# Kernel optimization log

Hardware: AMD Instinct MI355X
Metric: run time of the kernel (lower is better)

## Reference

```python
import jax, jax.numpy as jnp
import numpy as np

NUM_HEADS = 16
DIM_HEAD = 64
MAX_LEN = 512


def setup_inputs() -> dict:
    key = jax.random.key(0)
    ks = jax.random.split(key, 6)
    B, N, D = 16, 512, 1024
    inner = NUM_HEADS * DIM_HEAD  # 1024
    x = jax.random.normal(ks[0], (B, N, D), dtype=jnp.float32)
    w_qkv = jax.random.normal(ks[1], (D, 3 * inner), dtype=jnp.float32) * (D ** -0.5)
    b_qkv = jnp.zeros((3 * inner,), dtype=jnp.float32)
    rel_emb = jax.random.normal(ks[2], (2 * MAX_LEN - 1, NUM_HEADS), dtype=jnp.float32) * 0.02
    w_out = jax.random.normal(ks[3], (inner, D), dtype=jnp.float32) * (inner ** -0.5)
    b_out = jnp.zeros((D,), dtype=jnp.float32)
    return {"x": x, "w_qkv": w_qkv, "b_qkv": b_qkv, "rel_emb": rel_emb,
            "w_out": w_out, "b_out": b_out}


def reference(x, w_qkv, b_qkv, rel_emb, w_out, b_out):
    B, N, D = x.shape
    h, dh = NUM_HEADS, DIM_HEAD
    scale = dh ** -0.5
    qkv = x @ w_qkv + b_qkv  # (B, N, 3*h*dh)
    q, k, v = jnp.split(qkv, 3, axis=-1)
    def to_heads(t):
        return t.reshape(B, N, h, dh).transpose(0, 2, 1, 3)  # (B, h, N, dh)
    q, k, v = to_heads(q), to_heads(k), to_heads(v)
    dots = jnp.einsum('bhid,bhjd->bhij', q, k) * scale  # (B, h, N, N)
    # relative position bias: emb[(i - j) + max_len - 1] -> (N, N, h) -> (1, h, N, N)
    idx = jnp.arange(N)[:, None] - jnp.arange(N)[None, :] + (MAX_LEN - 1)
    bias = rel_emb[idx].transpose(2, 0, 1)[None]  # (1, h, N, N)
    attn = jax.nn.softmax(dots + bias, axis=-1)
    out = jnp.einsum('bhij,bhjd->bhid', attn, v)  # (B, h, N, dh)
    out = out.transpose(0, 2, 1, 3).reshape(B, N, h * dh)
    return out @ w_out + b_out
```

## Files before the change

### kernel.cpp

```cpp
#include <hip/hip_runtime.h>

#define SEQ    512
#define NH     16
#define DH     64
#define DMODEL 1024
#define NB     16
#define MROWS  (NB*SEQ)
#define MAXL   512

typedef _Float16 f16;
typedef f16  f16x8 __attribute__((ext_vector_type(8)));
typedef f16  f16x4 __attribute__((ext_vector_type(4)));
typedef float f32x4 __attribute__((ext_vector_type(4)));

__device__ static inline void gll16(const f16* g, f16* l) {
    __builtin_amdgcn_global_load_lds(
        (const __attribute__((address_space(1))) void*)(g),
        (__attribute__((address_space(3))) void*)(l), 16, 0, 0);
}

__global__ __launch_bounds__(256)
void prep(const float* __restrict__ x, f16* __restrict__ xh,
          const float* __restrict__ wqkv, f16* __restrict__ wqkvT,
          const float* __restrict__ wout, f16* __restrict__ woutT)
{
    const int bid = blockIdx.x, t = threadIdx.x;
    if (bid < 8192) {
        int i = (bid * 256 + t) * 4;
        float4 v = *(const float4*)(x + i);
        f16x4 h = { (f16)v.x, (f16)v.y, (f16)v.z, (f16)v.w };
        *(f16x4*)(xh + i) = h;
        return;
    }
    __shared__ float tile[32][33];
    const float* in; f16* out; int C, gx, gy;
    if (bid < 8192 + 3072) {
        int b2 = bid - 8192; in = wqkv; out = wqkvT; C = 3072;
        gx = b2 % 96; gy = b2 / 96;
    } else {
        int b2 = bid - 11264; in = wout; out = woutT; C = 1024;
        gx = b2 & 31; gy = b2 >> 5;
    }
    const int R = 1024;
    int tx = t & 31, ty = t >> 5;
    int c0 = gx * 32, r0 = gy * 32;
    #pragma unroll
    for (int i = 0; i < 4; ++i)
        tile[ty + i * 8][tx] = in[(size_t)(r0 + ty + i * 8) * C + c0 + tx];
    __syncthreads();
    #pragma unroll
    for (int i = 0; i < 4; ++i)
        out[(size_t)(c0 + ty + i * 8) * R + r0 + tx] = (f16)tile[tx][ty + i * 8];
}

template<int MODE>
__global__ __launch_bounds__(256)
void gemm_mfma(const f16* __restrict__ A, const f16* __restrict__ Bt,
               const float* __restrict__ bias, int N, int K,
               float* __restrict__ Cout,
               f16* __restrict__ qb, f16* __restrict__ kb, f16* __restrict__ vb)
{
    __shared__ f16 As[128 * 64];
    __shared__ f16 Bs[128 * 64];
    const int t = threadIdx.x;
    const int lane = t & 63, w = t >> 6;
    const int quad = lane >> 4, l16 = lane & 15;
    const int xr = l16 & 7;
    const int m0 = blockIdx.y * 128, n0 = blockIdx.x * 128;
    const int wm = (w & 1) * 64, wn = (w >> 1) * 64;

    f32x4 acc[4][4];
    #pragma unroll
    for (int i = 0; i < 4; ++i)
        #pragma unroll
        for (int j = 0; j < 4; ++j)
            acc[i][j] = f32x4{0.f, 0.f, 0.f, 0.f};

    const int sr8 = lane >> 3;
    const int sc8 = (lane & 7) ^ sr8;
    const f16* agp = A  + (size_t)(m0 + w * 32 + sr8) * K + sc8 * 8;
    const f16* bgp = Bt + (size_t)(n0 + w * 32 + sr8) * K + sc8 * 8;
    f16* asl = As + w * 2048;
    f16* bsl = Bs + w * 2048;

    for (int k0 = 0; k0 < K; k0 += 64) {
        __syncthreads();
        #pragma unroll
        for (int c = 0; c < 4; ++c) {
            gll16(agp + k0 + c * 8 * K, asl + c * 512);
            gll16(bgp + k0 + c * 8 * K, bsl + c * 512);
        }
        __syncthreads();
        #pragma unroll
        for (int ks = 0; ks < 2; ++ks) {
            f16x8 af[4], bf[4];
            #pragma unroll
            for (int ms = 0; ms < 4; ++ms)
                af[ms] = *(const f16x8*)&As[(wm + ms * 16 + l16) * 64
                                            + (((ks * 4 + quad) ^ xr) * 8)];
            #pragma unroll
            for (int ns = 0; ns < 4; ++ns)
                bf[ns] = *(const f16x8*)&Bs[(wn + ns * 16 + l16) * 64
                                            + (((ks * 4 + quad) ^ xr) * 8)];
            #pragma unroll
            for (int ms = 0; ms < 4; ++ms)
                #pragma unroll
                for (int ns = 0; ns < 4; ++ns)
                    acc[ms][ns] = __builtin_amdgcn_mfma_f32_16x16x32_f16(
                        af[ms], bf[ns], acc[ms][ns], 0, 0, 0);
        }
    }

    if (MODE == 0) {
        #pragma unroll
        for (int ns = 0; ns < 4; ++ns) {
            int col = n0 + wn + ns * 16 + l16;
            float bv = bias[col];
            int which = col >> 10;
            int hh = (col & 1023) >> 6, d = col & 63;
            #pragma unroll
            for (int ms = 0; ms < 4; ++ms) {
                int rowb = m0 + wm + ms * 16 + quad * 4;
                int bb_ = rowb >> 9, n_ = rowb & 511;
                if (which == 0) {
                    #pragma unroll
                    for (int reg = 0; reg < 4; ++reg)
                        qb[((size_t)(bb_ * NH + hh) * SEQ + n_ + reg) * DH + d] =
                            (f16)(acc[ms][ns][reg] + bv);
                } else if (which == 2) {
                    f16x4 pk;
                    #pragma unroll
                    for (int reg = 0; reg < 4; ++reg)
                        pk[reg] = (f16)(acc[ms][ns][reg] + bv);
                    int c8s = ((n_ >> 3) & 7) ^ (d & 7);
                    *(f16x4*)(vb + ((size_t)(bb_ * NH + hh) * DH + d) * SEQ
                                 + (n_ & ~63) + c8s * 8 + (n_ & 7)) = pk;
                } else {
                    #pragma unroll
                    for (int reg = 0; reg < 4; ++reg) {
                        int n = n_ + reg;
                        int dd = (((d >> 3) ^ (n & 7)) * 8) + (d & 7);
                        kb[((size_t)(bb_ * NH + hh) * SEQ + n) * DH + dd] =
                            (f16)(acc[ms][ns][reg] + bv);
                    }
                }
            }
        }
    } else {
        #pragma unroll
        for (int ns = 0; ns < 4; ++ns) {
            int col = n0 + wn + ns * 16 + l16;
            float bv = bias[col];
            #pragma unroll
            for (int ms = 0; ms < 4; ++ms) {
                int rowb = m0 + wm + ms * 16 + quad * 4;
                #pragma unroll
                for (int reg = 0; reg < 4; ++reg)
                    Cout[(size_t)(rowb + reg) * N + col] = acc[ms][ns][reg] + bv;
            }
        }
    }
}

__global__ __launch_bounds__(512)
void attn_mfma(const f16* __restrict__ qb, const f16* __restrict__ kb,
               const f16* __restrict__ vb, const float* __restrict__ rel,
               f16* __restrict__ ob)
{
    __shared__ f16 Ks[128 * 64];
    __shared__ f16 Vt[64 * 128];
    __shared__ f16 Pw[8][16 * 64];
    __shared__ float relh[1024];

    const int t = threadIdx.x;
    const int lane = t & 63, w = t >> 6;
    const int quad = lane >> 4, l16 = lane & 15;
    const int xr = l16 & 7;
    const int bh = blockIdx.x;
    const int h = bh & 15, b = bh >> 4;

    for (int i = t; i < 2 * MAXL - 1; i += 512)
        relh[i] = rel[i * NH + h] * 1.44269504f;

    f16x8 qf[4][2];
    #pragma unroll
    for (int c = 0; c < 4; ++c) {
        const f16* qrow = qb + ((size_t)bh * SEQ + w * 64 + c * 16 + l16) * DH + quad * 8;
        qf[c][0] = *(const f16x8*)(qrow);
        qf[c][1] = *(const f16x8*)(qrow + 32);
    }

    f32x4 o[4][4];
    float lsum[4];
    #pragma unroll
    for (int c = 0; c < 4; ++c) {
        lsum[c] = 0.f;
        #pragma unroll
        for (int dt = 0; dt < 4; ++dt) o[c][dt] = f32x4{0.f, 0.f, 0.f, 0.f};
    }

    const f16* kbase = kb + (size_t)bh * SEQ * DH;
    const f16* vbase = vb + (size_t)bh * DH * SEQ;
    f16* pw = &Pw[w][0];

    for (int kt = 0; kt < 4; ++kt) {
        __syncthreads();
        #pragma unroll
        for (int r = 0; r < 2; ++r) {
            const f16* src = kbase + (size_t)(kt * 128 + r * 64 + w * 8 + (lane >> 3)) * DH
                           + (lane & 7) * 8;
            gll16(src, Ks + r * 4096 + w * 512);
        }
        #pragma unroll
        for (int r = 0; r < 2; ++r) {
            const f16* src = vbase + (size_t)(r * 32 + w * 4 + (lane >> 4)) * SEQ
                           + kt * 128 + ((lane & 15) >> 3) * 64 + (lane & 7) * 8;
            gll16(src, Vt + r * 4096 + w * 512);
        }
        __syncthreads();

        #pragma unroll
        for (int c = 0; c < 4; ++c) {
            f32x4 sT[8];
            #pragma unroll
            for (int mt = 0; mt < 8; ++mt) {
                const f16* kr = &Ks[(mt * 16 + l16) * 64];
                f16x8 a0 = *(const f16x8*)(kr + ((quad ^ xr) * 8));
                f16x8 a1 = *(const f16x8*)(kr + (((4 + quad) ^ xr) * 8));
                f32x4 s = f32x4{0.f, 0.f, 0.f, 0.f};
                s = __builtin_amdgcn_mfma_f32_16x16x32_f16(a0, qf[c][0], s, 0, 0, 0);
                s = __builtin_amdgcn_mfma_f32_16x16x32_f16(a1, qf[c][1], s, 0, 0, 0);
                sT[mt] = s;
            }

            const int cb0 = w * 64 + c * 16 + l16 + (MAXL - 1) - kt * 128 - quad * 4;
            #pragma unroll
            for (int g = 0; g < 2; ++g) {
                #pragma unroll
                for (int m4 = 0; m4 < 4; ++m4) {
                    int mt = g * 4 + m4;
                    f16x4 pk;
                    #pragma unroll
                    for (int reg = 0; reg < 4; ++reg) {
                        float e = exp2f(fmaf(sT[mt][reg], 0.180336878f,
                                             relh[cb0 - mt * 16 - reg]));
                        lsum[c] += e;
                        pk[reg] = (f16)e;
                    }
                    int c8 = (m4 * 2 + (quad >> 1)) ^ xr;
                    *(f16x4*)&pw[l16 * 64 + c8 * 8 + (quad & 1) * 4] = pk;
                }
                __builtin_amdgcn_s_waitcnt(0xC07F);

                #pragma unroll
                for (int s2 = 0; s2 < 2; ++s2) {
                    f16x8 pa = *(const f16x8*)&pw[l16 * 64 + (((s2 * 4 + quad) ^ xr) * 8)];
                    #pragma unroll
                    for (int dt = 0; dt < 4; ++dt) {
                        const f16* vr = &Vt[(dt * 16 + l16) * 128 + g * 64];
                        f16x8 vb8 = *(const f16x8*)(vr + (((s2 * 4 + quad) ^ xr) * 8));
                        o[c][dt] = __builtin_amdgcn_mfma_f32_16x16x32_f16(
                            pa, vb8, o[c][dt], 0, 0, 0);
                    }
                }
            }
        }
    }

    #pragma unroll
    for (int c = 0; c < 4; ++c) {
        float ls = lsum[c];
        ls += __shfl_xor(ls, 16, 64);
        ls += __shfl_xor(ls, 32, 64);
        #pragma unroll
        for (int reg = 0; reg < 4; ++reg) {
            float inv = 1.0f / __shfl(ls, quad * 4 + reg, 64);
            size_t rbase = ((size_t)b * SEQ + w * 64 + c * 16 + quad * 4 + reg) * DMODEL
                         + h * DH;
            #pragma unroll
            for (int dt = 0; dt < 4; ++dt)
                ob[rbase + dt * 16 + l16] = (f16)(o[c][dt][reg] * inv);
        }
    }
}

extern "C" void kernel_launch(void* const* d_in, const int* in_sizes, int n_in,
                              void* d_out, int out_size, void* d_ws, size_t ws_size,
                              hipStream_t stream)
{
    const float* x    = (const float*)d_in[0];
    const float* wqkv = (const float*)d_in[1];
    const float* bqkv = (const float*)d_in[2];
    const float* rel  = (const float*)d_in[3];
    const float* wout = (const float*)d_in[4];
    const float* bout = (const float*)d_in[5];
    float* out = (float*)d_out;
    char* ws = (char*)d_ws;

    const size_t XH = (size_t)MROWS * DMODEL;
    f16* xh    = (f16*)(ws);
    f16* wqkvT = (f16*)(ws + 2 * XH);
    f16* woutT = wqkvT + (size_t)3 * DMODEL * DMODEL;
    f16* qbuf  = woutT + (size_t)DMODEL * DMODEL;
    f16* kbuf  = qbuf + XH;
    f16* vbuf  = kbuf + XH;
    f16* abuf  = vbuf + XH;

    prep<<<12288, 256, 0, stream>>>(x, xh, wqkv, wqkvT, wout, woutT);

    gemm_mfma<0><<<dim3(3 * DMODEL / 128, MROWS / 128), 256, 0, stream>>>(
        xh, wqkvT, bqkv, 3 * DMODEL, DMODEL, nullptr, qbuf, kbuf, vbuf);

    attn_mfma<<<NB * NH, 512, 0, stream>>>(qbuf, kbuf, vbuf, rel, abuf);

    gemm_mfma<1><<<dim3(DMODEL / 128, MROWS / 128), 256, 0, stream>>>(
        abuf, woutT, bout, DMODEL, DMODEL, out, nullptr, nullptr, nullptr);
}
```

Measured before the change: 230.1 us.

## Split attention queries across two blocks and double-buffer K/V tiles

```diff
diff --git a/kernel.cpp b/kernel.cpp
--- a/kernel.cpp
+++ b/kernel.cpp
@@ -162,30 +162,33 @@
     }
 }
 
-__global__ __launch_bounds__(512)
+__global__ __launch_bounds__(256, 2)
 void attn_mfma(const f16* __restrict__ qb, const f16* __restrict__ kb,
                const f16* __restrict__ vb, const float* __restrict__ rel,
                f16* __restrict__ ob)
 {
-    __shared__ f16 Ks[128 * 64];
-    __shared__ f16 Vt[64 * 128];
-    __shared__ f16 Pw[8][16 * 64];
+    __shared__ f16 Ks[2][128 * 64];
+    __shared__ f16 Vt[2][64 * 128];
+    __shared__ f16 Pw[4][16 * 64];
     __shared__ float relh[1024];
 
     const int t = threadIdx.x;
     const int lane = t & 63, w = t >> 6;
     const int quad = lane >> 4, l16 = lane & 15;
     const int xr = l16 & 7;
-    const int bh = blockIdx.x;
+    const int bid = blockIdx.x;
+    const int bh = bid & 255, halfq = bid >> 8;
     const int h = bh & 15, b = bh >> 4;
-
-    for (int i = t; i < 2 * MAXL - 1; i += 512)
+    const int q0 = halfq * 256;
+
+    for (int i = t; i < 2 * MAXL - 1; i += 256)
         relh[i] = rel[i * NH + h] * 1.44269504f;
 
     f16x8 qf[4][2];
     #pragma unroll
     for (int c = 0; c < 4; ++c) {
-        const f16* qrow = qb + ((size_t)bh * SEQ + w * 64 + c * 16 + l16) * DH + quad * 8;
+        const f16* qrow = qb + ((size_t)bh * SEQ + q0 + w * 64 + c * 16 + l16) * DH
+                        + quad * 8;
         qf[c][0] = *(const f16x8*)(qrow);
         qf[c][1] = *(const f16x8*)(qrow + 32);
     }
@@ -203,28 +206,37 @@
     const f16* vbase = vb + (size_t)bh * DH * SEQ;
     f16* pw = &Pw[w][0];
 
+    auto stage = [&](int kt, int buf) {
+        #pragma unroll
+        for (int r = 0; r < 4; ++r) {
+            const f16* src = kbase
+                + (size_t)(kt * 128 + r * 32 + w * 8 + (lane >> 3)) * DH
+                + (lane & 7) * 8;
+            gll16(src, Ks[buf] + r * 2048 + w * 512);
+        }
+        #pragma unroll
+        for (int r = 0; r < 4; ++r) {
+            const f16* src = vbase
+                + (size_t)(r * 16 + w * 4 + (lane >> 4)) * SEQ
+                + kt * 128 + ((lane >> 3) & 1) * 64 + (lane & 7) * 8;
+            gll16(src, Vt[buf] + r * 2048 + w * 512);
+        }
+    };
+
+    stage(0, 0);
+    __syncthreads();
+
     for (int kt = 0; kt < 4; ++kt) {
-        __syncthreads();
-        #pragma unroll
-        for (int r = 0; r < 2; ++r) {
-            const f16* src = kbase + (size_t)(kt * 128 + r * 64 + w * 8 + (lane >> 3)) * DH
-                           + (lane & 7) * 8;
-            gll16(src, Ks + r * 4096 + w * 512);
-        }
-        #pragma unroll
-        for (int r = 0; r < 2; ++r) {
-            const f16* src = vbase + (size_t)(r * 32 + w * 4 + (lane >> 4)) * SEQ
-                           + kt * 128 + ((lane & 15) >> 3) * 64 + (lane & 7) * 8;
-            gll16(src, Vt + r * 4096 + w * 512);
-        }
-        __syncthreads();
+        if (kt < 3) stage(kt + 1, (kt + 1) & 1);
+        const f16* ks = Ks[kt & 1];
+        const f16* vt = Vt[kt & 1];
 
         #pragma unroll
         for (int c = 0; c < 4; ++c) {
             f32x4 sT[8];
             #pragma unroll
             for (int mt = 0; mt < 8; ++mt) {
-                const f16* kr = &Ks[(mt * 16 + l16) * 64];
+                const f16* kr = &ks[(mt * 16 + l16) * 64];
                 f16x8 a0 = *(const f16x8*)(kr + ((quad ^ xr) * 8));
                 f16x8 a1 = *(const f16x8*)(kr + (((4 + quad) ^ xr) * 8));
                 f32x4 s = f32x4{0.f, 0.f, 0.f, 0.f};
@@ -233,7 +245,8 @@
                 sT[mt] = s;
             }
 
-            const int cb0 = w * 64 + c * 16 + l16 + (MAXL - 1) - kt * 128 - quad * 4;
+            const int cb0 = q0 + w * 64 + c * 16 + l16 + (MAXL - 1)
+                          - kt * 128 - quad * 4;
             #pragma unroll
             for (int g = 0; g < 2; ++g) {
                 #pragma unroll
@@ -257,7 +270,7 @@
                     f16x8 pa = *(const f16x8*)&pw[l16 * 64 + (((s2 * 4 + quad) ^ xr) * 8)];
                     #pragma unroll
                     for (int dt = 0; dt < 4; ++dt) {
-                        const f16* vr = &Vt[(dt * 16 + l16) * 128 + g * 64];
+                        const f16* vr = &vt[(dt * 16 + l16) * 128 + g * 64];
                         f16x8 vb8 = *(const f16x8*)(vr + (((s2 * 4 + quad) ^ xr) * 8));
                         o[c][dt] = __builtin_amdgcn_mfma_f32_16x16x32_f16(
                             pa, vb8, o[c][dt], 0, 0, 0);
@@ -265,6 +278,7 @@
                 }
             }
         }
+        __syncthreads();
     }
 
     #pragma unroll
@@ -275,8 +289,8 @@
         #pragma unroll
         for (int reg = 0; reg < 4; ++reg) {
             float inv = 1.0f / __shfl(ls, quad * 4 + reg, 64);
-            size_t rbase = ((size_t)b * SEQ + w * 64 + c * 16 + quad * 4 + reg) * DMODEL
-                         + h * DH;
+            size_t rbase = ((size_t)b * SEQ + q0 + w * 64 + c * 16 + quad * 4 + reg)
+                         * DMODEL + h * DH;
             #pragma unroll
             for (int dt = 0; dt < 4; ++dt)
                 ob[rbase + dt * 16 + l16] = (f16)(o[c][dt][reg] * inv);
@@ -311,7 +325,7 @@
     gemm_mfma<0><<<dim3(3 * DMODEL / 128, MROWS / 128), 256, 0, stream>>>(
         xh, wqkvT, bqkv, 3 * DMODEL, DMODEL, nullptr, qbuf, kbuf, vbuf);
 
-    attn_mfma<<<NB * NH, 512, 0, stream>>>(qbuf, kbuf, vbuf, rel, abuf);
+    attn_mfma<<<2 * NB * NH, 256, 0, stream>>>(qbuf, kbuf, vbuf, rel, abuf);
 
     gemm_mfma<1><<<dim3(DMODEL / 128, MROWS / 128), 256, 0, stream>>>(
         abuf, woutT, bout, DMODEL, DMODEL, out, nullptr, nullptr, nullptr);
```

Measured after the change: 237.5 us. 3.2% more time.

## Process query chunks in pairs to reuse K/V fragments; precompute relative bias in prep

Applied to the files above, without the earlier changes.

```diff
diff --git a/kernel.cpp b/kernel.cpp
--- a/kernel.cpp
+++ b/kernel.cpp
@@ -22,23 +22,35 @@
 __global__ __launch_bounds__(256)
 void prep(const float* __restrict__ x, f16* __restrict__ xh,
           const float* __restrict__ wqkv, f16* __restrict__ wqkvT,
-          const float* __restrict__ wout, f16* __restrict__ woutT)
+          const float* __restrict__ wout, f16* __restrict__ woutT,
+          const float* __restrict__ rel, float* __restrict__ rel2)
 {
     const int bid = blockIdx.x, t = threadIdx.x;
-    if (bid < 8192) {
-        int i = (bid * 256 + t) * 4;
-        float4 v = *(const float4*)(x + i);
-        f16x4 h = { (f16)v.x, (f16)v.y, (f16)v.z, (f16)v.w };
-        *(f16x4*)(xh + i) = h;
+    if (bid < 1024) {
+        const int S = 1024 * 256 * 4;
+        int i0 = (bid * 256 + t) * 4;
+        #pragma unroll
+        for (int k = 0; k < 8; ++k) {
+            int i = i0 + k * S;
+            float4 v = *(const float4*)(x + i);
+            f16x4 hh = { (f16)v.x, (f16)v.y, (f16)v.z, (f16)v.w };
+            *(f16x4*)(xh + i) = hh;
+        }
+        return;
+    }
+    if (bid >= 5120) {
+        int h = bid - 5120;
+        for (int i = t; i < 2 * MAXL - 1; i += 256)
+            rel2[h * 1024 + i] = rel[i * NH + h] * 1.44269504f;
         return;
     }
     __shared__ float tile[32][33];
     const float* in; f16* out; int C, gx, gy;
-    if (bid < 8192 + 3072) {
-        int b2 = bid - 8192; in = wqkv; out = wqkvT; C = 3072;
+    if (bid < 4096) {
+        int b2 = bid - 1024; in = wqkv; out = wqkvT; C = 3072;
         gx = b2 % 96; gy = b2 / 96;
     } else {
-        int b2 = bid - 11264; in = wout; out = woutT; C = 1024;
+        int b2 = bid - 4096; in = wout; out = woutT; C = 1024;
         gx = b2 & 31; gy = b2 >> 5;
     }
     const int R = 1024;
@@ -162,15 +174,14 @@
     }
 }
 
-__global__ __launch_bounds__(512)
+__global__ __launch_bounds__(512, 2)
 void attn_mfma(const f16* __restrict__ qb, const f16* __restrict__ kb,
-               const f16* __restrict__ vb, const float* __restrict__ rel,
+               const f16* __restrict__ vb, const float* __restrict__ rel2,
                f16* __restrict__ ob)
 {
     __shared__ f16 Ks[128 * 64];
     __shared__ f16 Vt[64 * 128];
-    __shared__ f16 Pw[8][16 * 64];
-    __shared__ float relh[1024];
+    __shared__ f16 Pw[8][2][16 * 64];
 
     const int t = threadIdx.x;
     const int lane = t & 63, w = t >> 6;
@@ -178,9 +189,7 @@
     const int xr = l16 & 7;
     const int bh = blockIdx.x;
     const int h = bh & 15, b = bh >> 4;
-
-    for (int i = t; i < 2 * MAXL - 1; i += 512)
-        relh[i] = rel[i * NH + h] * 1.44269504f;
+    const float* r2 = rel2 + h * 1024;
 
     f16x8 qf[4][2];
     #pragma unroll
@@ -201,7 +210,6 @@
 
     const f16* kbase = kb + (size_t)bh * SEQ * DH;
     const f16* vbase = vb + (size_t)bh * DH * SEQ;
-    f16* pw = &Pw[w][0];
 
     for (int kt = 0; kt < 4; ++kt) {
         __syncthreads();
@@ -214,53 +222,68 @@
         #pragma unroll
         for (int r = 0; r < 2; ++r) {
             const f16* src = vbase + (size_t)(r * 32 + w * 4 + (lane >> 4)) * SEQ
-                           + kt * 128 + ((lane & 15) >> 3) * 64 + (lane & 7) * 8;
+                           + kt * 128 + ((lane >> 3) & 1) * 64 + (lane & 7) * 8;
             gll16(src, Vt + r * 4096 + w * 512);
         }
         __syncthreads();
 
         #pragma unroll
-        for (int c = 0; c < 4; ++c) {
-            f32x4 sT[8];
+        for (int cp = 0; cp < 2; ++cp) {
+            f32x4 sT[2][8];
             #pragma unroll
             for (int mt = 0; mt < 8; ++mt) {
                 const f16* kr = &Ks[(mt * 16 + l16) * 64];
                 f16x8 a0 = *(const f16x8*)(kr + ((quad ^ xr) * 8));
                 f16x8 a1 = *(const f16x8*)(kr + (((4 + quad) ^ xr) * 8));
-                f32x4 s = f32x4{0.f, 0.f, 0.f, 0.f};
-                s = __builtin_amdgcn_mfma_f32_16x16x32_f16(a0, qf[c][0], s, 0, 0, 0);
-                s = __builtin_amdgcn_mfma_f32_16x16x32_f16(a1, qf[c][1], s, 0, 0, 0);
-                sT[mt] = s;
+                #pragma unroll
+                for (int cc = 0; cc < 2; ++cc) {
+                    f32x4 s = f32x4{0.f, 0.f, 0.f, 0.f};
+                    s = __builtin_amdgcn_mfma_f32_16x16x32_f16(a0, qf[cp * 2 + cc][0], s, 0, 0, 0);
+                    s = __builtin_amdgcn_mfma_f32_16x16x32_f16(a1, qf[cp * 2 + cc][1], s, 0, 0, 0);
+                    sT[cc][mt] = s;
+                }
             }
 
-            const int cb0 = w * 64 + c * 16 + l16 + (MAXL - 1) - kt * 128 - quad * 4;
             #pragma unroll
             for (int g = 0; g < 2; ++g) {
                 #pragma unroll
-                for (int m4 = 0; m4 < 4; ++m4) {
-                    int mt = g * 4 + m4;
-                    f16x4 pk;
-                    #pragma unroll
-                    for (int reg = 0; reg < 4; ++reg) {
-                        float e = exp2f(fmaf(sT[mt][reg], 0.180336878f,
-                                             relh[cb0 - mt * 16 - reg]));
-                        lsum[c] += e;
-                        pk[reg] = (f16)e;
+                for (int cc = 0; cc < 2; ++cc) {
+                    const int c = cp * 2 + cc;
+                    const int cb0 = w * 64 + c * 16 + l16 + (MAXL - 1) - kt * 128 - quad * 4;
+                    f16* pw = &Pw[w][cc][0];
+                    #pragma unroll
+                    for (int m4 = 0; m4 < 4; ++m4) {
+                        int mt = g * 4 + m4;
+                        f16x4 pk;
+                        #pragma unroll
+                        for (int reg = 0; reg < 4; ++reg) {
+                            float e = exp2f(fmaf(sT[cc][mt][reg], 0.180336878f,
+                                                 r2[cb0 - mt * 16 - reg]));
+                            lsum[c] += e;
+                            pk[reg] = (f16)e;
+                        }
+                        int c8 = (m4 * 2 + (quad >> 1)) ^ xr;
+                        *(f16x4*)&pw[l16 * 64 + c8 * 8 + (quad & 1) * 4] = pk;
                     }
-                    int c8 = (m4 * 2 + (quad >> 1)) ^ xr;
-                    *(f16x4*)&pw[l16 * 64 + c8 * 8 + (quad & 1) * 4] = pk;
                 }
                 __builtin_amdgcn_s_waitcnt(0xC07F);
 
                 #pragma unroll
                 for (int s2 = 0; s2 < 2; ++s2) {
-                    f16x8 pa = *(const f16x8*)&pw[l16 * 64 + (((s2 * 4 + quad) ^ xr) * 8)];
-                    #pragma unroll
-                    for (int dt = 0; dt < 4; ++dt) {
-                        const f16* vr = &Vt[(dt * 16 + l16) * 128 + g * 64];
-                        f16x8 vb8 = *(const f16x8*)(vr + (((s2 * 4 + quad) ^ xr) * 8));
-                        o[c][dt] = __builtin_amdgcn_mfma_f32_16x16x32_f16(
-                            pa, vb8, o[c][dt], 0, 0, 0);
+                    f16x8 vf[4];
+                    #pragma unroll
+                    for (int dt = 0; dt < 4; ++dt)
+                        vf[dt] = *(const f16x8*)&Vt[(dt * 16 + l16) * 128 + g * 64
+                                                    + (((s2 * 4 + quad) ^ xr) * 8)];
+                    #pragma unroll
+                    for (int cc = 0; cc < 2; ++cc) {
+                        const int c = cp * 2 + cc;
+                        f16x8 pa = *(const f16x8*)&Pw[w][cc][l16 * 64
+                                                    + (((s2 * 4 + quad) ^ xr) * 8)];
+                        #pragma unroll
+                        for (int dt = 0; dt < 4; ++dt)
+                            o[c][dt] = __builtin_amdgcn_mfma_f32_16x16x32_f16(
+                                pa, vf[dt], o[c][dt], 0, 0, 0);
                     }
                 }
             }
@@ -305,13 +328,14 @@
     f16* kbuf  = qbuf + XH;
     f16* vbuf  = kbuf + XH;
     f16* abuf  = vbuf + XH;
-
-    prep<<<12288, 256, 0, stream>>>(x, xh, wqkv, wqkvT, wout, woutT);
+    float* rel2 = (float*)(abuf + XH);
+
+    prep<<<5136, 256, 0, stream>>>(x, xh, wqkv, wqkvT, wout, woutT, rel, rel2);
 
     gemm_mfma<0><<<dim3(3 * DMODEL / 128, MROWS / 128), 256, 0, stream>>>(
         xh, wqkvT, bqkv, 3 * DMODEL, DMODEL, nullptr, qbuf, kbuf, vbuf);
 
-    attn_mfma<<<NB * NH, 512, 0, stream>>>(qbuf, kbuf, vbuf, rel, abuf);
+    attn_mfma<<<NB * NH, 512, 0, stream>>>(qbuf, kbuf, vbuf, rel2, abuf);
 
     gemm_mfma<1><<<dim3(DMODEL / 128, MROWS / 128), 256, 0, stream>>>(
         abuf, woutT, bout, DMODEL, DMODEL, out, nullptr, nullptr, nullptr);
```

After: 307.0 us. +33.5%, slower.
